# Optimization experiments

Hardware: AMD Instinct MI355X
Metric: run time of the kernel (lower is better)

The kernel has to match this reference:

```python
import math
import jax, jax.numpy as jnp
import numpy as np

N_STEPS = 5
STEP = 0.1      # step_size buffer (eval mode: never updated)
LMBD = 0.1
MU = 0.0
N_DICT = 1


def _prox(c):
    # elasnet_prox: softshrink(c * s_mu, lmbd*step * s_mu); with mu=0, s_mu=1
    s_mu = 1.0 / (1.0 + MU * STEP)
    lam = LMBD * STEP * s_mu
    c = c * s_mu
    return jnp.sign(c) * jnp.maximum(jnp.abs(c) - lam, 0.0)


def _fista(x, W):
    # x: [N, C], W: [D, C]; F.linear(x, W) == x @ W.T
    s = STEP
    # i == 0
    c = jax.nn.relu(_prox(s * (x @ W.T)))
    # i == 1
    c_pre = c
    r = x - c @ W                      # residual [N, C]
    c = jax.nn.relu(_prox(c + s * (r @ W.T)))
    t = (math.sqrt(5.0) + 1.0) / 2.0
    # i >= 2: FISTA momentum, gradient evaluated at c (as in source)
    for _ in range(2, N_STEPS):
        t_pre = t
        t = (math.sqrt(1.0 + 4.0 * t_pre * t_pre) + 1.0) / 2.0
        a = (t_pre + t - 1.0) / t * c + (1.0 - t_pre) / t * c_pre
        c_pre = c
        r = x - c @ W
        c = jax.nn.relu(_prox(a + s * (r @ W.T)))
    return c


def setup_inputs() -> dict:
    key = jax.random.key(0)
    k1, k2 = jax.random.split(key)
    x = jax.random.normal(k1, (8, 2048, 512), dtype=jnp.float32)
    # kaiming-uniform-like dictionary [dict_size, n_channel]
    bound = math.sqrt(6.0 / 512.0)
    weight = jax.random.uniform(k2, (2048, 512), dtype=jnp.float32,
                                minval=-bound, maxval=bound)
    return {"x": x, "weight": weight}


def reference(x, weight):
    bs, tok, dim = x.shape
    xf = x.reshape(-1, dim)                    # [N, C]
    c = _fista(xf, weight)                     # [N, D]
    xp = c @ weight                            # [N, C]
    r = xf - xp
    r_loss = jnp.sum(r * r) / N_DICT
    c_loss = LMBD * jnp.sum(jnp.abs(c)) + 0.5 * MU * jnp.sum(c * c)
    return (c.reshape(bs, tok, -1), xp.reshape(bs, tok, -1), r, r_loss, c_loss)
```

## Files before the change

### kernel.cpp

```cpp
#include <hip/hip_runtime.h>
#include <cmath>


typedef __attribute__((ext_vector_type(8))) short bf16x8;
typedef __attribute__((ext_vector_type(8))) unsigned short u16x8;
typedef __attribute__((ext_vector_type(4))) float f32x4;

constexpr float S_STEP = 0.1f;
constexpr float LAM    = 0.01f;

__device__ __forceinline__ unsigned short f2bf(float f) {
    unsigned u = __float_as_uint(f);
    u += 0x7FFFu + ((u >> 16) & 1u);
    return (unsigned short)(u >> 16);
}
__device__ __forceinline__ float bf2f(unsigned short s) {
    return __uint_as_float(((unsigned)s) << 16);
}

__device__ __forceinline__ void async16(const void* g, void* l) {
    __builtin_amdgcn_global_load_lds(
        (const __attribute__((address_space(1))) void*)g,
        (__attribute__((address_space(3))) void*)l, 16, 0, 0);
}

template<int EPI>
__global__ __launch_bounds__(256)
void gemm_bt(const short* __restrict__ A, const short* __restrict__ B,
             int K, int Nn, int lbx,
             const unsigned short* Cc, const unsigned short* Cpre,
             const unsigned short* __restrict__ Xb,
             unsigned short* OutB, float* Out32,
             float cfA, float cfB, float* loss)
{
    __shared__ __align__(16) unsigned char smem[32768];
    short* S  = (short*)smem;
    float (*L)[132] = (float (*)[132])smem;
    float* red2 = (float*)(smem + 32736);

    const int tid  = threadIdx.x;
    const int wave = tid >> 6;
    const int lane = tid & 63;

    const int qchunk = gridDim.x >> 3;
    const int idx    = (blockIdx.x & 7) * qchunk + (blockIdx.x >> 3);
    const int rowBase = (idx >> lbx) * 128;
    const int colBase = (idx & ((1 << lbx) - 1)) * 128;

    const int sRow = lane >> 2;
    const int sK   = (lane & 3) << 3;
    const short* gA = A + (size_t)(rowBase + wave * 32 + sRow) * K + sK;
    const short* gB = B + (size_t)(colBase + wave * 32 + sRow) * K + sK;
    const size_t rstep = (size_t)16 * K;
    short* lA = S + (wave * 32) * 32;
    short* lB = S + 8192 + (wave * 32) * 32;

    const int m16  = lane & 15;
    const int quad = lane >> 4;
    const short* paBase = S + ((wave & 1) * 64 + m16) * 32 + quad * 8;
    const short* pbBase = S + 8192 + ((wave >> 1) * 64 + m16) * 32 + quad * 8;

    f32x4 acc[4][4] = {};
    const int nIter = K >> 5;

    {
        async16(gA,         lA);
        async16(gA + rstep, lA + 512);
        async16(gB,         lB);
        async16(gB + rstep, lB + 512);
    }

    for (int it = 0; it < nIter; ++it) {
        __syncthreads();
        if (it + 1 < nIter) {
            const int nb = (it + 1) & 1;
            const int kb = (it + 1) << 5;
            async16(gA + kb,         lA + nb * 4096);
            async16(gA + kb + rstep, lA + nb * 4096 + 512);
            async16(gB + kb,         lB + nb * 4096);
            async16(gB + kb + rstep, lB + nb * 4096 + 512);
        }
        const int cb = (it & 1) * 4096;
        bf16x8 af[4], bfr[4];
        #pragma unroll
        for (int i = 0; i < 4; ++i) af[i]  = *(const bf16x8*)(paBase + cb + i * 512);
        #pragma unroll
        for (int j = 0; j < 4; ++j) bfr[j] = *(const bf16x8*)(pbBase + cb + j * 512);
        #pragma unroll
        for (int i = 0; i < 4; ++i)
            #pragma unroll
            for (int j = 0; j < 4; ++j)
                acc[i][j] = __builtin_amdgcn_mfma_f32_16x16x32_bf16(
                                af[i], bfr[j], acc[i][j], 0, 0, 0);
    }

    const int lrow = tid >> 3;
    const int seg  = tid & 7;
    const bool useCp = (cfB != 0.f);
    float lsum = 0.f;

    #pragma unroll
    for (int t = 0; t < 4; ++t) {
        __syncthreads();
        if ((wave & 1) == (t >> 1)) {
            #pragma unroll
            for (int ii = 0; ii < 2; ++ii) {
                const int i   = (t & 1) * 2 + ii;
                const int lr0 = ii * 16 + quad * 4;
                #pragma unroll
                for (int r = 0; r < 4; ++r)
                    #pragma unroll
                    for (int j = 0; j < 4; ++j)
                        L[lr0 + r][(wave >> 1) * 64 + j * 16 + m16] = acc[i][j][r];
            }
        }
        __syncthreads();

        float v[16];
        #pragma unroll
        for (int q = 0; q < 4; ++q)
            *(f32x4*)&v[q * 4] = *(const f32x4*)&L[lrow][seg * 16 + q * 4];

        const size_t gidx = (size_t)(rowBase + t * 32 + lrow) * Nn
                          + colBase + seg * 16;

        if constexpr (EPI == 0) {
            u16x8 o0, o1;
            #pragma unroll
            for (int k = 0; k < 8; ++k) {
                o0[k] = f2bf(fmaxf(S_STEP * v[k]     - LAM, 0.f));
                o1[k] = f2bf(fmaxf(S_STEP * v[k + 8] - LAM, 0.f));
            }
            *(u16x8*)(OutB + gidx)     = o0;
            *(u16x8*)(OutB + gidx + 8) = o1;
        } else if constexpr (EPI == 1 || EPI == 2) {
            const u16x8 cc0 = *(const u16x8*)(Cc   + gidx);
            const u16x8 cc1 = *(const u16x8*)(Cc   + gidx + 8);
            u16x8 cp0 = {}, cp1 = {};
            if (useCp) {
                cp0 = *(const u16x8*)(Cpre + gidx);
                cp1 = *(const u16x8*)(Cpre + gidx + 8);
            }
            float w[16];
            #pragma unroll
            for (int k = 0; k < 8; ++k) {
                w[k]     = fmaxf(cfA * bf2f(cc0[k]) + cfB * bf2f(cp0[k])
                                 + S_STEP * v[k]     - LAM, 0.f);
                w[k + 8] = fmaxf(cfA * bf2f(cc1[k]) + cfB * bf2f(cp1[k])
                                 + S_STEP * v[k + 8] - LAM, 0.f);
            }
            u16x8 o0, o1;
            #pragma unroll
            for (int k = 0; k < 8; ++k) { o0[k] = f2bf(w[k]); o1[k] = f2bf(w[k + 8]); }
            *(u16x8*)(OutB + gidx)     = o0;
            *(u16x8*)(OutB + gidx + 8) = o1;
            if constexpr (EPI == 2) {
                #pragma unroll
                for (int q = 0; q < 4; ++q)
                    *(f32x4*)(Out32 + gidx + q * 4) = *(const f32x4*)&w[q * 4];
                #pragma unroll
                for (int k = 0; k < 16; ++k) lsum += w[k];
            }
        } else if constexpr (EPI == 3) {
            const u16x8 xb0 = *(const u16x8*)(Xb + gidx);
            const u16x8 xb1 = *(const u16x8*)(Xb + gidx + 8);
            u16x8 o0, o1;
            #pragma unroll
            for (int k = 0; k < 8; ++k) {
                o0[k] = f2bf(bf2f(xb0[k]) - v[k]);
                o1[k] = f2bf(bf2f(xb1[k]) - v[k + 8]);
            }
            *(u16x8*)(OutB + gidx)     = o0;
            *(u16x8*)(OutB + gidx + 8) = o1;
        } else {
            #pragma unroll
            for (int q = 0; q < 4; ++q)
                *(f32x4*)(Out32 + gidx + q * 4) = *(const f32x4*)&v[q * 4];
        }
    }

    if constexpr (EPI == 2) {
        #pragma unroll
        for (int off = 32; off; off >>= 1) lsum += __shfl_down(lsum, off, 64);
        if (lane == 0) red2[wave] = lsum;
        __syncthreads();
        if (tid == 0)
            atomicAdd(loss, 0.1f * (red2[0] + red2[1] + red2[2] + red2[3]));
    }
}

__global__ __launch_bounds__(256)
void cvt_w_k(const float* __restrict__ W,
             unsigned short* __restrict__ Wb, unsigned short* __restrict__ Wtb)
{
    __shared__ unsigned short T[64][65];
    const int dBase = blockIdx.y * 64;
    const int cBase = blockIdx.x * 64;
    const int lc = threadIdx.x & 63;
    const int lr = threadIdx.x >> 6;
    #pragma unroll
    for (int p = 0; p < 16; ++p) {
        const int dl = p * 4 + lr;
        const size_t idx = (size_t)(dBase + dl) * 512 + cBase + lc;
        const unsigned short b = f2bf(W[idx]);
        Wb[idx] = b;
        T[dl][lc] = b;
    }
    __syncthreads();
    #pragma unroll
    for (int p = 0; p < 16; ++p) {
        const int cl = p * 4 + lr;
        Wtb[(size_t)(cBase + cl) * 2048 + dBase + lc] = T[lc][cl];
    }
}

__global__ __launch_bounds__(256)
void cvt_x_k(const float4* __restrict__ x4, ushort4* __restrict__ xb4, int n4)
{
    for (int i = blockIdx.x * 256 + threadIdx.x; i < n4; i += gridDim.x * 256) {
        const float4 v = x4[i];
        xb4[i] = make_ushort4(f2bf(v.x), f2bf(v.y), f2bf(v.z), f2bf(v.w));
    }
}

__global__ __launch_bounds__(256)
void finalize_k(const float4* __restrict__ x4, const float4* __restrict__ xp4,
                float4* __restrict__ r4, float* __restrict__ rloss, int n4)
{
    float lsum = 0.f;
    for (int i = blockIdx.x * 256 + threadIdx.x; i < n4; i += gridDim.x * 256) {
        const float4 xv = x4[i], pv = xp4[i];
        float4 rv;
        rv.x = xv.x - pv.x; rv.y = xv.y - pv.y;
        rv.z = xv.z - pv.z; rv.w = xv.w - pv.w;
        r4[i] = rv;
        lsum += rv.x * rv.x + rv.y * rv.y + rv.z * rv.z + rv.w * rv.w;
    }
    #pragma unroll
    for (int off = 32; off; off >>= 1) lsum += __shfl_down(lsum, off, 64);
    if ((threadIdx.x & 63) == 0) atomicAdd(rloss, lsum);
}

extern "C" void kernel_launch(void* const* d_in, const int* in_sizes, int n_in,
                              void* d_out, int out_size, void* d_ws, size_t ws_size,
                              hipStream_t stream)
{
    (void)in_sizes; (void)n_in; (void)out_size; (void)ws_size;

    constexpr int N = 16384, C = 512, D = 2048;
    constexpr size_t ND = (size_t)N * D;
    constexpr size_t NC = (size_t)N * C;

    const float* x = (const float*)d_in[0];
    const float* W = (const float*)d_in[1];

    float* out    = (float*)d_out;
    float* c_out  = out;
    float* xp_out = out + ND;
    float* r_out  = out + ND + NC;
    float* rloss  = out + ND + 2 * NC;
    float* closs  = rloss + 1;

    short* cb0 = (short*)d_ws;
    short* cb1 = cb0 + ND;

    unsigned short* rb  = (unsigned short*)xp_out;
    unsigned short* Wb  = (unsigned short*)xp_out + NC;
    unsigned short* Wtb = (unsigned short*)r_out;
    unsigned short* xb  = (unsigned short*)r_out + (size_t)D * C;

    hipMemsetAsync((void*)rloss, 0, 2 * sizeof(float), stream);

    double tp = (std::sqrt(5.0) + 1.0) / 2.0;
    float cfA[5] = {0.f, 1.f, 0.f, 0.f, 0.f};
    float cfB[5] = {0.f, 0.f, 0.f, 0.f, 0.f};
    for (int i = 2; i < 5; ++i) {
        double t = (std::sqrt(1.0 + 4.0 * tp * tp) + 1.0) / 2.0;
        cfA[i] = (float)((tp + t - 1.0) / t);
        cfB[i] = (float)((1.0 - tp) / t);
        tp = t;
    }

    const dim3 blk(256);
    cvt_w_k<<<dim3(C / 64, D / 64), blk, 0, stream>>>(W, Wb, Wtb);
    cvt_x_k<<<dim3(1024), blk, 0, stream>>>((const float4*)x, (ushort4*)xb,
                                            (int)(NC / 4));

    const dim3 gridD((D / 128) * (N / 128));
    const dim3 gridC((C / 128) * (N / 128));
    constexpr int LBX_D = 4, LBX_C = 2;

    gemm_bt<0><<<gridD, blk, 0, stream>>>((const short*)xb, (const short*)Wb,
                                          C, D, LBX_D, nullptr, nullptr, nullptr,
                                          (unsigned short*)cb0, nullptr,
                                          0.f, 0.f, nullptr);

    short* bufs[2] = {cb0, cb1};
    for (int i = 1; i < 5; ++i) {
        const short* cprev = bufs[(i - 1) & 1];
        short*       cnew  = bufs[i & 1];
        const unsigned short* cpre2 =
            (i == 1) ? (const unsigned short*)cprev : (const unsigned short*)cnew;
        gemm_bt<3><<<gridC, blk, 0, stream>>>(cprev, (const short*)Wtb,
                                              D, C, LBX_C, nullptr, nullptr, xb,
                                              rb, nullptr, 0.f, 0.f, nullptr);
        if (i < 4)
            gemm_bt<1><<<gridD, blk, 0, stream>>>((const short*)rb, (const short*)Wb,
                                                  C, D, LBX_D,
                                                  (const unsigned short*)cprev,
                                                  cpre2, nullptr,
                                                  (unsigned short*)cnew, nullptr,
                                                  cfA[i], cfB[i], nullptr);
        else
            gemm_bt<2><<<gridD, blk, 0, stream>>>((const short*)rb, (const short*)Wb,
                                                  C, D, LBX_D,
                                                  (const unsigned short*)cprev,
                                                  cpre2, nullptr,
                                                  (unsigned short*)cnew, c_out,
                                                  cfA[i], cfB[i], closs);
    }

    gemm_bt<4><<<gridC, blk, 0, stream>>>(cb0, (const short*)Wtb,
                                          D, C, LBX_C, nullptr, nullptr, nullptr,
                                          nullptr, xp_out, 0.f, 0.f, nullptr);

    finalize_k<<<dim3(1024), blk, 0, stream>>>((const float4*)x,
                                               (const float4*)xp_out,
                                               (float4*)r_out, rloss,
                                               (int)(NC / 4));
}
```

Before: 760.2 us.

## Fuse residual and loss into final GEMM epilogue and prefetch epilogue operands

Removes the separate finalize kernel by computing r = x - xp and the squared-residual loss inside the last GEMM's epilogue, which avoids re-reading xp and x from global memory. Epilogue global loads (c, c_pre, xb, x) for the next 32-row slice are issued before the current slice is processed, so their latency overlaps with compute. It also adds a kernel that copies Wtb into the cb1 buffer and uses that copy as the B operand for the final GEMM, which costs an extra launch and a 2 MB copy for no clear reason. Prefetching keeps two sets of operand registers live, which raises register pressure.

```diff
diff --git a/kernel.cpp b/kernel.cpp
--- a/kernel.cpp
+++ b/kernel.cpp
@@ -29,8 +29,8 @@
 void gemm_bt(const short* __restrict__ A, const short* __restrict__ B,
              int K, int Nn, int lbx,
              const unsigned short* Cc, const unsigned short* Cpre,
-             const unsigned short* __restrict__ Xb,
-             unsigned short* OutB, float* Out32,
+             const unsigned short* __restrict__ Xb, const float* __restrict__ Xf,
+             unsigned short* OutB, float* Out32, float* R32,
              float cfA, float cfB, float* loss)
 {
     __shared__ __align__(16) unsigned char smem[32768];
@@ -99,6 +99,26 @@
     const bool useCp = (cfB != 0.f);
     float lsum = 0.f;
 
+    auto gofs = [&](int t) -> size_t {
+        return (size_t)(rowBase + t * 32 + lrow) * Nn + colBase + seg * 16;
+    };
+
+    u16x8 cc0{}, cc1{}, cp0{}, cp1{}, xq0{}, xq1{};
+    float xfv[16];
+    if constexpr (EPI == 1 || EPI == 2) {
+        const size_t g = gofs(0);
+        cc0 = *(const u16x8*)(Cc + g); cc1 = *(const u16x8*)(Cc + g + 8);
+        if (useCp) { cp0 = *(const u16x8*)(Cpre + g); cp1 = *(const u16x8*)(Cpre + g + 8); }
+    } else if constexpr (EPI == 3) {
+        const size_t g = gofs(0);
+        xq0 = *(const u16x8*)(Xb + g); xq1 = *(const u16x8*)(Xb + g + 8);
+    } else if constexpr (EPI == 4) {
+        const size_t g = gofs(0);
+        #pragma unroll
+        for (int q = 0; q < 4; ++q)
+            *(f32x4*)&xfv[q * 4] = *(const f32x4*)(Xf + g + q * 4);
+    }
+
     #pragma unroll
     for (int t = 0; t < 4; ++t) {
         __syncthreads();
@@ -121,8 +141,23 @@
         for (int q = 0; q < 4; ++q)
             *(f32x4*)&v[q * 4] = *(const f32x4*)&L[lrow][seg * 16 + q * 4];
 
-        const size_t gidx = (size_t)(rowBase + t * 32 + lrow) * Nn
-                          + colBase + seg * 16;
+        const size_t gidx = gofs(t);
+
+        u16x8 ncc0{}, ncc1{}, ncp0{}, ncp1{}, nxq0{}, nxq1{};
+        float nxfv[16];
+        if (t < 3) {
+            const size_t gn = gofs(t + 1);
+            if constexpr (EPI == 1 || EPI == 2) {
+                ncc0 = *(const u16x8*)(Cc + gn); ncc1 = *(const u16x8*)(Cc + gn + 8);
+                if (useCp) { ncp0 = *(const u16x8*)(Cpre + gn); ncp1 = *(const u16x8*)(Cpre + gn + 8); }
+            } else if constexpr (EPI == 3) {
+                nxq0 = *(const u16x8*)(Xb + gn); nxq1 = *(const u16x8*)(Xb + gn + 8);
+            } else if constexpr (EPI == 4) {
+                #pragma unroll
+                for (int q = 0; q < 4; ++q)
+                    *(f32x4*)&nxfv[q * 4] = *(const f32x4*)(Xf + gn + q * 4);
+            }
+        }
 
         if constexpr (EPI == 0) {
             u16x8 o0, o1;
@@ -134,13 +169,6 @@
             *(u16x8*)(OutB + gidx)     = o0;
             *(u16x8*)(OutB + gidx + 8) = o1;
         } else if constexpr (EPI == 1 || EPI == 2) {
-            const u16x8 cc0 = *(const u16x8*)(Cc   + gidx);
-            const u16x8 cc1 = *(const u16x8*)(Cc   + gidx + 8);
-            u16x8 cp0 = {}, cp1 = {};
-            if (useCp) {
-                cp0 = *(const u16x8*)(Cpre + gidx);
-                cp1 = *(const u16x8*)(Cpre + gidx + 8);
-            }
             float w[16];
             #pragma unroll
             for (int k = 0; k < 8; ++k) {
@@ -162,30 +190,50 @@
                 for (int k = 0; k < 16; ++k) lsum += w[k];
             }
         } else if constexpr (EPI == 3) {
-            const u16x8 xb0 = *(const u16x8*)(Xb + gidx);
-            const u16x8 xb1 = *(const u16x8*)(Xb + gidx + 8);
             u16x8 o0, o1;
             #pragma unroll
             for (int k = 0; k < 8; ++k) {
-                o0[k] = f2bf(bf2f(xb0[k]) - v[k]);
-                o1[k] = f2bf(bf2f(xb1[k]) - v[k + 8]);
+                o0[k] = f2bf(bf2f(xq0[k]) - v[k]);
+                o1[k] = f2bf(bf2f(xq1[k]) - v[k + 8]);
             }
             *(u16x8*)(OutB + gidx)     = o0;
             *(u16x8*)(OutB + gidx + 8) = o1;
         } else {
-            #pragma unroll
-            for (int q = 0; q < 4; ++q)
+            float rv[16];
+            #pragma unroll
+            for (int k = 0; k < 16; ++k) {
+                rv[k] = xfv[k] - v[k];
+                lsum += rv[k] * rv[k];
+            }
+            #pragma unroll
+            for (int q = 0; q < 4; ++q) {
                 *(f32x4*)(Out32 + gidx + q * 4) = *(const f32x4*)&v[q * 4];
-        }
-    }
-
-    if constexpr (EPI == 2) {
+                *(f32x4*)(R32   + gidx + q * 4) = *(const f32x4*)&rv[q * 4];
+            }
+        }
+
+        if (t < 3) {
+            if constexpr (EPI == 1 || EPI == 2) {
+                cc0 = ncc0; cc1 = ncc1;
+                if (useCp) { cp0 = ncp0; cp1 = ncp1; }
+            } else if constexpr (EPI == 3) {
+                xq0 = nxq0; xq1 = nxq1;
+            } else if constexpr (EPI == 4) {
+                #pragma unroll
+                for (int k = 0; k < 16; ++k) xfv[k] = nxfv[k];
+            }
+        }
+    }
+
+    if constexpr (EPI == 2 || EPI == 4) {
         #pragma unroll
         for (int off = 32; off; off >>= 1) lsum += __shfl_down(lsum, off, 64);
         if (lane == 0) red2[wave] = lsum;
         __syncthreads();
-        if (tid == 0)
-            atomicAdd(loss, 0.1f * (red2[0] + red2[1] + red2[2] + red2[3]));
+        if (tid == 0) {
+            const float s = red2[0] + red2[1] + red2[2] + red2[3];
+            atomicAdd(loss, (EPI == 2) ? 0.1f * s : s);
+        }
     }
 }
 
@@ -224,21 +272,10 @@
 }
 
 __global__ __launch_bounds__(256)
-void finalize_k(const float4* __restrict__ x4, const float4* __restrict__ xp4,
-                float4* __restrict__ r4, float* __restrict__ rloss, int n4)
-{
-    float lsum = 0.f;
-    for (int i = blockIdx.x * 256 + threadIdx.x; i < n4; i += gridDim.x * 256) {
-        const float4 xv = x4[i], pv = xp4[i];
-        float4 rv;
-        rv.x = xv.x - pv.x; rv.y = xv.y - pv.y;
-        rv.z = xv.z - pv.z; rv.w = xv.w - pv.w;
-        r4[i] = rv;
-        lsum += rv.x * rv.x + rv.y * rv.y + rv.z * rv.z + rv.w * rv.w;
-    }
-    #pragma unroll
-    for (int off = 32; off; off >>= 1) lsum += __shfl_down(lsum, off, 64);
-    if ((threadIdx.x & 63) == 0) atomicAdd(rloss, lsum);
+void copy_wtb_k(const u16x8* __restrict__ src, u16x8* __restrict__ dst)
+{
+    const int i = blockIdx.x * 256 + threadIdx.x;
+    dst[i] = src[i];
 }
 
 extern "C" void kernel_launch(void* const* d_in, const int* in_sizes, int n_in,
@@ -291,8 +328,9 @@
     constexpr int LBX_D = 4, LBX_C = 2;
 
     gemm_bt<0><<<gridD, blk, 0, stream>>>((const short*)xb, (const short*)Wb,
-                                          C, D, LBX_D, nullptr, nullptr, nullptr,
-                                          (unsigned short*)cb0, nullptr,
+                                          C, D, LBX_D, nullptr, nullptr,
+                                          nullptr, nullptr,
+                                          (unsigned short*)cb0, nullptr, nullptr,
                                           0.f, 0.f, nullptr);
 
     short* bufs[2] = {cb0, cb1};
@@ -302,30 +340,31 @@
         const unsigned short* cpre2 =
             (i == 1) ? (const unsigned short*)cprev : (const unsigned short*)cnew;
         gemm_bt<3><<<gridC, blk, 0, stream>>>(cprev, (const short*)Wtb,
-                                              D, C, LBX_C, nullptr, nullptr, xb,
-                                              rb, nullptr, 0.f, 0.f, nullptr);
+                                              D, C, LBX_C, nullptr, nullptr,
+                                              xb, nullptr,
+                                              rb, nullptr, nullptr,
+                                              0.f, 0.f, nullptr);
         if (i < 4)
             gemm_bt<1><<<gridD, blk, 0, stream>>>((const short*)rb, (const short*)Wb,
                                                   C, D, LBX_D,
                                                   (const unsigned short*)cprev,
-                                                  cpre2, nullptr,
+                                                  cpre2, nullptr, nullptr,
                                                   (unsigned short*)cnew, nullptr,
-                                                  cfA[i], cfB[i], nullptr);
+                                                  nullptr, cfA[i], cfB[i], nullptr);
         else
             gemm_bt<2><<<gridD, blk, 0, stream>>>((const short*)rb, (const short*)Wb,
                                                   C, D, LBX_D,
                                                   (const unsigned short*)cprev,
-                                                  cpre2, nullptr,
+                                                  cpre2, nullptr, nullptr,
                                                   (unsigned short*)cnew, c_out,
-                                                  cfA[i], cfB[i], closs);
-    }
-
-    gemm_bt<4><<<gridC, blk, 0, stream>>>(cb0, (const short*)Wtb,
-                                          D, C, LBX_C, nullptr, nullptr, nullptr,
-                                          nullptr, xp_out, 0.f, 0.f, nullptr);
-
-    finalize_k<<<dim3(1024), blk, 0, stream>>>((const float4*)x,
-                                               (const float4*)xp_out,
-                                               (float4*)r_out, rloss,
-                                               (int)(NC / 4));
-}
+                                                  nullptr, cfA[i], cfB[i], closs);
+    }
+
+    copy_wtb_k<<<dim3(512), blk, 0, stream>>>((const u16x8*)Wtb, (u16x8*)cb1);
+
+    gemm_bt<4><<<gridC, blk, 0, stream>>>(cb0, (const short*)cb1,
+                                          D, C, LBX_C, nullptr, nullptr,
+                                          nullptr, x,
+                                          nullptr, xp_out, r_out,
+                                          0.f, 0.f, rloss);
+}
```

New measurement: 745.7 us. No clear change (-1.9%).
